# Kernel tuning notes

Hardware: AMD Instinct MI355X
Metric: run time of the kernel (lower is better)

The kernel has to match this reference:

```python
import jax, jax.numpy as jnp
import numpy as np

B, S, HID = 1, 2048, 2048
NH, NKV, D = 32, 8, 64
GROUPS = NH // NKV
THETA = 10000.0


def _rope_tables(seq_len, dim):
    inv_freq = 1.0 / (THETA ** (jnp.arange(0, dim, 2, dtype=jnp.float32) / dim))
    t = jnp.arange(seq_len, dtype=jnp.float32)
    freqs = jnp.outer(t, inv_freq)            # [S, D/2]
    emb = jnp.concatenate([freqs, freqs], axis=-1)  # [S, D]
    return jnp.cos(emb), jnp.sin(emb)


def _rotate_half(x):
    x1, x2 = jnp.split(x, 2, axis=-1)
    return jnp.concatenate([-x2, x1], axis=-1)


def setup_inputs() -> dict:
    key = jax.random.key(0)
    ks = jax.random.split(key, 8)
    hidden_states = jax.random.normal(ks[0], (B, S, HID), dtype=jnp.float32)
    # additive causal mask, 0 on/below diagonal, -1e9 above
    causal = jnp.tril(jnp.ones((S, S), dtype=bool))
    attention_mask = jnp.where(causal, 0.0, -1e9).astype(jnp.float32)[None, None]
    sc = 0.02
    Wq = sc * jax.random.normal(ks[1], (NH * D, HID), dtype=jnp.float32)
    bq = jnp.zeros((NH * D,), dtype=jnp.float32)
    Wk = sc * jax.random.normal(ks[2], (NKV * D, HID), dtype=jnp.float32)
    bk = jnp.zeros((NKV * D,), dtype=jnp.float32)
    Wv = sc * jax.random.normal(ks[3], (NKV * D, HID), dtype=jnp.float32)
    bv = jnp.zeros((NKV * D,), dtype=jnp.float32)
    Wo = sc * jax.random.normal(ks[4], (HID, NH * D), dtype=jnp.float32)
    return {"hidden_states": hidden_states, "attention_mask": attention_mask,
            "Wq": Wq, "bq": bq, "Wk": Wk, "bk": bk, "Wv": Wv, "bv": bv, "Wo": Wo}


def reference(hidden_states, attention_mask, Wq, bq, Wk, bk, Wv, bv, Wo):
    b, s, _ = hidden_states.shape
    q = (hidden_states @ Wq.T + bq).reshape(b, s, NH, D).transpose(0, 2, 1, 3)   # [B,NH,S,D]
    k = (hidden_states @ Wk.T + bk).reshape(b, s, NKV, D).transpose(0, 2, 1, 3)  # [B,NKV,S,D]
    v = (hidden_states @ Wv.T + bv).reshape(b, s, NKV, D).transpose(0, 2, 1, 3)
    cos, sin = _rope_tables(s, D)
    cos = cos[None, None]; sin = sin[None, None]
    q = q * cos + _rotate_half(q) * sin
    k = k * cos + _rotate_half(k) * sin
    # GQA: repeat KV heads to match query heads
    k = jnp.repeat(k, GROUPS, axis=1)  # [B,NH,S,D]
    v = jnp.repeat(v, GROUPS, axis=1)
    scores = jnp.einsum('bhqd,bhkd->bhqk', q, k) / jnp.sqrt(jnp.float32(D))
    scores = jnp.clip(scores, -50.0, 50.0)
    scores = scores + attention_mask
    probs = jax.nn.softmax(scores.astype(jnp.float32), axis=-1).astype(q.dtype)
    attn = jnp.einsum('bhqk,bhkd->bhqd', probs, v)
    attn = attn.transpose(0, 2, 1, 3).reshape(b, s, NH * D)
    return attn @ Wo.T
```

## Files before the change

### kernel.cpp

```cpp
#include <hip/hip_runtime.h>
#include <hip/hip_bf16.h>
#include <stdint.h>

typedef unsigned short u16;
typedef unsigned int u32;

#define S_LEN 2048
#define HID 2048
#define NH 32
#define NKV 8
#define HD 64
#define PIT 2080

using f32x4 = __attribute__((ext_vector_type(4))) float;
using bfrag = __attribute__((ext_vector_type(8))) short;

__device__ __forceinline__ float b2f(u16 u) {
  union { u32 i; float f; } c; c.i = ((u32)u) << 16; return c.f;
}
__device__ __forceinline__ u16 f2b(float f) {
  union { float f; u32 i; } c; c.f = f;
  u32 r = c.i + 0x7fffu + ((c.i >> 16) & 1u);
  return (u16)(r >> 16);
}
__device__ __forceinline__ uint4 cvt8(const float* __restrict__ p) {
  float4 a = *(const float4*)p;
  float4 b = *(const float4*)(p + 4);
  uint4 r;
  r.x = (u32)f2b(a.x) | ((u32)f2b(a.y) << 16);
  r.y = (u32)f2b(a.z) | ((u32)f2b(a.w) << 16);
  r.z = (u32)f2b(b.x) | ((u32)f2b(b.y) << 16);
  r.w = (u32)f2b(b.z) | ((u32)f2b(b.w) << 16);
  return r;
}

__device__ __forceinline__ void gl2lds16(const u16* g, u16* l) {
  __builtin_amdgcn_global_load_lds(
      (const __attribute__((address_space(1))) void*)g,
      (__attribute__((address_space(3))) void*)l,
      16, 0, 0);
}

#define WAITBAR(N) asm volatile("s_waitcnt vmcnt(" #N ")\ns_barrier" ::: "memory")

__global__ void conv_all(const float* __restrict__ hid, const float* __restrict__ Wq,
                         const float* __restrict__ Wk, const float* __restrict__ Wv,
                         u16* __restrict__ hidb, u16* __restrict__ Wqkvb) {
  int row = blockIdx.x;
  int col = threadIdx.x * 8;
  const float* src; u16* dst;
  if (row < 2048)      { src = hid + (size_t)row * 2048;          dst = hidb  + (size_t)row * PIT; }
  else if (row < 4096) { src = Wq + (size_t)(row - 2048) * 2048;  dst = Wqkvb + (size_t)(row - 2048) * PIT; }
  else if (row < 4608) { src = Wk + (size_t)(row - 4096) * 2048;  dst = Wqkvb + (size_t)(row - 4096 + 2048) * PIT; }
  else                 { src = Wv + (size_t)(row - 4608) * 2048;  dst = Wqkvb + (size_t)(row - 4608 + 2560) * PIT; }
  *(uint4*)(dst + col) = cvt8(src + col);
}

__global__ void conv_f2b_p(const float* __restrict__ in, u16* __restrict__ out, int n8) {
  int i = blockIdx.x * 256 + threadIdx.x;
  if (i >= n8) return;
  int row = i >> 8;
  int col = (i & 255) * 8;
  *(uint4*)(out + (size_t)row * PIT + col) = cvt8(in + (size_t)row * 2048 + col);
}

__global__ __launch_bounds__(256, 3) void gemm_qkv(
    const u16* __restrict__ A, const u16* __restrict__ B,
    const float* __restrict__ bq, const float* __restrict__ bk, const float* __restrict__ bv,
    u16* __restrict__ Qb, u16* __restrict__ Kb, u16* __restrict__ Vt)
{
  __shared__ __align__(16) u16 As[3 * 2048];
  __shared__ __align__(16) u16 Bs[3 * 4096];
  __shared__ __align__(16) u16 strip_s[4][16 * 72];

  const int tid  = threadIdx.x;
  const int m0   = blockIdx.y * 64;
  const int n0   = blockIdx.x * 128;
  const int lane = tid & 63;
  const int w    = tid >> 6;
  const int wm   = w >> 1, wn = w & 1;
  const int quad = lane >> 4, l16 = lane & 15;

  const int srow = tid >> 2;
  const int scol = (tid & 3) * 8;
  const u16* ga = A + (size_t)(m0 + srow) * PIT + scol;
  const u16* gb = B + (size_t)(n0 + srow) * PIT + scol;

#define STAGE_G(bi, k0)                                                         \
  do {                                                                          \
    gl2lds16(ga + (k0), As + (bi) * 2048 + tid * 8);                            \
    gl2lds16(gb + (k0), Bs + (bi) * 4096 + tid * 8);                            \
    gl2lds16(gb + (size_t)64 * PIT + (k0), Bs + (bi) * 4096 + 2048 + tid * 8);  \
  } while (0)

  f32x4 zero = {0.f, 0.f, 0.f, 0.f};
  f32x4 acc[2][4];
#pragma unroll
  for (int mi = 0; mi < 2; ++mi)
#pragma unroll
    for (int ni = 0; ni < 4; ++ni) acc[mi][ni] = zero;

  STAGE_G(0, 0);
  STAGE_G(1, 32);

  int cur = 0;
  for (int k = 0; k < 64; ++k) {
    if (k < 63) WAITBAR(3);
    else        WAITBAR(0);
    if (k + 2 < 64) {
      int nb = cur + 2; if (nb >= 3) nb -= 3;
      STAGE_G(nb, (k + 2) * 32);
    }
    const u16* as = As + cur * 2048;
    const u16* bs = Bs + cur * 4096;

    bfrag af[2], bf[4];
#pragma unroll
    for (int i = 0; i < 2; ++i)
      af[i] = *(const bfrag*)&as[(wm * 32 + i * 16 + l16) * 32 + quad * 8];
#pragma unroll
    for (int i = 0; i < 4; ++i)
      bf[i] = *(const bfrag*)&bs[(wn * 64 + i * 16 + l16) * 32 + quad * 8];
#pragma unroll
    for (int mi = 0; mi < 2; ++mi)
#pragma unroll
      for (int ni = 0; ni < 4; ++ni)
        acc[mi][ni] = __builtin_amdgcn_mfma_f32_16x16x32_bf16(af[mi], bf[ni], acc[mi][ni], 0, 0, 0);

    cur += 1; if (cur == 3) cur = 0;
  }
#undef STAGE_G

  u16* strip = strip_s[w];
  const int rr = lane >> 2;
  const int co = (lane & 3) * 8;

  if (n0 < 2048) {
#pragma unroll
    for (int mi = 0; mi < 2; ++mi) {
#pragma unroll
      for (int n01 = 0; n01 < 2; ++n01)
#pragma unroll
        for (int i = 0; i < 4; ++i) {
          int d  = n01 * 16 + l16;
          int c1 = n0 + wn * 64 + d;
          float x1 = acc[mi][n01][i]     + bq[c1];
          float x2 = acc[mi][n01 + 2][i] + bq[c1 + 32];
          float inv = exp2f(-(float)d * 0.41524101186092034f);
          float ang = (float)(m0 + wm * 32 + mi * 16 + quad * 4 + i) * inv;
          float cs = cosf(ang), sn = sinf(ang);
          strip[(quad * 4 + i) * 72 + d]      = f2b(x1 * cs - x2 * sn);
          strip[(quad * 4 + i) * 72 + d + 32] = f2b(x2 * cs + x1 * sn);
        }
      uint4 v0 = *(const uint4*)&strip[rr * 72 + co];
      uint4 v1 = *(const uint4*)&strip[rr * 72 + 32 + co];
      size_t gb2 = (size_t)(m0 + wm * 32 + mi * 16 + rr) * 2048 + n0 + wn * 64;
      *(uint4*)(Qb + gb2 + co)      = v0;
      *(uint4*)(Qb + gb2 + 32 + co) = v1;
    }
  } else if (n0 < 2560) {
    int cb = (n0 - 2048) + wn * 64;
#pragma unroll
    for (int mi = 0; mi < 2; ++mi) {
#pragma unroll
      for (int n01 = 0; n01 < 2; ++n01)
#pragma unroll
        for (int i = 0; i < 4; ++i) {
          int d  = n01 * 16 + l16;
          int cg = cb + d;
          float x1 = acc[mi][n01][i]     + bk[cg];
          float x2 = acc[mi][n01 + 2][i] + bk[cg + 32];
          float inv = exp2f(-(float)d * 0.41524101186092034f);
          float ang = (float)(m0 + wm * 32 + mi * 16 + quad * 4 + i) * inv;
          float cs = cosf(ang), sn = sinf(ang);
          strip[(quad * 4 + i) * 72 + d]      = f2b(x1 * cs - x2 * sn);
          strip[(quad * 4 + i) * 72 + d + 32] = f2b(x2 * cs + x1 * sn);
        }
      uint4 v0 = *(const uint4*)&strip[rr * 72 + co];
      uint4 v1 = *(const uint4*)&strip[rr * 72 + 32 + co];
      size_t gb2 = (size_t)(m0 + wm * 32 + mi * 16 + rr) * 512 + cb;
      *(uint4*)(Kb + gb2 + co)      = v0;
      *(uint4*)(Kb + gb2 + 32 + co) = v1;
    }
  } else {
    int cgb = (n0 - 2560) + wn * 64;
#pragma unroll
    for (int ni = 0; ni < 4; ++ni) {
      float bvv = bv[cgb + ni * 16 + l16];
#pragma unroll
      for (int mi = 0; mi < 2; ++mi)
#pragma unroll
        for (int i = 0; i < 4; ++i)
          strip[l16 * 72 + mi * 16 + quad * 4 + i] = f2b(acc[mi][ni][i] + bvv);
      uint4 v0 = *(const uint4*)&strip[rr * 72 + co];
      size_t gb2 = (size_t)(cgb + ni * 16 + rr) * PIT + m0 + wm * 32;
      *(uint4*)(Vt + gb2 + co) = v0;
    }
  }
}

__global__ __launch_bounds__(256, 3) void gemm_o(
    const u16* __restrict__ A, const u16* __restrict__ B, float* __restrict__ C)
{
  __shared__ __align__(16) u16 As[3 * 2048];
  __shared__ __align__(16) u16 Bs[3 * 4096];

  const int tid  = threadIdx.x;
  const int m0   = blockIdx.y * 64;
  const int n0   = blockIdx.x * 128;
  const int lane = tid & 63;
  const int w    = tid >> 6;
  const int wm   = w >> 1, wn = w & 1;
  const int quad = lane >> 4, l16 = lane & 15;

  const int srow = tid >> 2;
  const int scol = (tid & 3) * 8;
  const u16* ga = A + (size_t)(m0 + srow) * PIT + scol;
  const u16* gb = B + (size_t)(n0 + srow) * PIT + scol;

#define STAGE_G(bi, k0)                                                         \
  do {                                                                          \
    gl2lds16(ga + (k0), As + (bi) * 2048 + tid * 8);                            \
    gl2lds16(gb + (k0), Bs + (bi) * 4096 + tid * 8);                            \
    gl2lds16(gb + (size_t)64 * PIT + (k0), Bs + (bi) * 4096 + 2048 + tid * 8);  \
  } while (0)

  f32x4 zero = {0.f, 0.f, 0.f, 0.f};
  f32x4 acc[2][4];
#pragma unroll
  for (int mi = 0; mi < 2; ++mi)
#pragma unroll
    for (int ni = 0; ni < 4; ++ni) acc[mi][ni] = zero;

  STAGE_G(0, 0);
  STAGE_G(1, 32);

  int cur = 0;
  for (int k = 0; k < 64; ++k) {
    if (k < 63) WAITBAR(3);
    else        WAITBAR(0);
    if (k + 2 < 64) {
      int nb = cur + 2; if (nb >= 3) nb -= 3;
      STAGE_G(nb, (k + 2) * 32);
    }
    const u16* as = As + cur * 2048;
    const u16* bs = Bs + cur * 4096;

    bfrag af[2], bf[4];
#pragma unroll
    for (int i = 0; i < 2; ++i)
      af[i] = *(const bfrag*)&as[(wm * 32 + i * 16 + l16) * 32 + quad * 8];
#pragma unroll
    for (int i = 0; i < 4; ++i)
      bf[i] = *(const bfrag*)&bs[(wn * 64 + i * 16 + l16) * 32 + quad * 8];
#pragma unroll
    for (int mi = 0; mi < 2; ++mi)
#pragma unroll
      for (int ni = 0; ni < 4; ++ni)
        acc[mi][ni] = __builtin_amdgcn_mfma_f32_16x16x32_bf16(af[mi], bf[ni], acc[mi][ni], 0, 0, 0);

    cur += 1; if (cur == 3) cur = 0;
  }
#undef STAGE_G

#pragma unroll
  for (int ni = 0; ni < 4; ++ni) {
    int col = n0 + wn * 64 + ni * 16 + l16;
#pragma unroll
    for (int mi = 0; mi < 2; ++mi)
#pragma unroll
      for (int i = 0; i < 4; ++i) {
        int row = m0 + wm * 32 + mi * 16 + quad * 4 + i;
        C[(size_t)row * 2048 + col] = acc[mi][ni][i];
      }
  }
}

#define SM_SC 0.18033688011112042f
#define SM_UB 72.134752044448169f

__global__ __launch_bounds__(256, 2) void attn_flash5(
    const u16* __restrict__ Qb, const u16* __restrict__ Kb,
    const u16* __restrict__ Vt, u16* __restrict__ Ab)
{
  __shared__ __align__(16) u16 Ks[3][64 * 64];
  __shared__ __align__(16) u16 Vs[3][64 * 64];
  __shared__ __align__(16) u16 Ps[4][2][16][72];

  const int h    = blockIdx.x;
  const int qbb  = 15 - (int)blockIdx.y;
  const int kvh  = h >> 2;
  const int tid  = threadIdx.x;
  const int lane = tid & 63;
  const int w    = tid >> 6;
  const int quad = lane >> 4, l16 = lane & 15;

  const int c0  = w * 128 + lane;
  const int r0  = c0 >> 3,        s0 = c0 & 7;
  const int r1  = (c0 + 64) >> 3, s1 = (c0 + 64) & 7;
  const int sg0 = s0 ^ (r0 & 7);
  const int sg1 = s1 ^ (r1 & 7);
  const u16* Ksrc0 = Kb + (size_t)r0 * 512 + kvh * 64 + sg0 * 8;
  const u16* Ksrc1 = Kb + (size_t)r1 * 512 + kvh * 64 + sg1 * 8;
  const u16* Vsrc0 = Vt + (size_t)(kvh * 64 + r0) * PIT + sg0 * 8;
  const u16* Vsrc1 = Vt + (size_t)(kvh * 64 + r1) * PIT + sg1 * 8;

#define STAGEKV(buf, kb)                                                        \
  do {                                                                          \
    gl2lds16(Ksrc0 + (size_t)(kb) * 32768, &Ks[buf][0] + c0 * 8);               \
    gl2lds16(Ksrc1 + (size_t)(kb) * 32768, &Ks[buf][0] + (c0 + 64) * 8);        \
    gl2lds16(Vsrc0 + (kb) * 64,            &Vs[buf][0] + c0 * 8);               \
    gl2lds16(Vsrc1 + (kb) * 64,            &Vs[buf][0] + (c0 + 64) * 8);        \
  } while (0)

  const int bulk  = 2 * qbb;
  const int kbmax = bulk + 1;

  STAGEKV(0, 0);
  STAGEKV(1, 1);

  bfrag qf[2][2];
#pragma unroll
  for (int g = 0; g < 2; ++g) {
    const u16* qp = Qb + (size_t)(qbb * 128 + g * 64 + w * 16 + l16) * 2048 + h * 64 + quad * 8;
    qf[g][0] = *(const bfrag*)qp;
    qf[g][1] = *(const bfrag*)(qp + 32);
  }

  f32x4 zero = {0.f, 0.f, 0.f, 0.f};
  f32x4 o_acc[2][4];
  float lpart[2][4];
#pragma unroll
  for (int g = 0; g < 2; ++g)
#pragma unroll
    for (int nb = 0; nb < 4; ++nb) { o_acc[g][nb] = zero; lpart[g][nb] = 0.f; }

#define QKT_SM_FULL(g)                                                          \
  do {                                                                          \
    f32x4 s_acc[4];                                                             \
    _Pragma("unroll")                                                           \
    for (int nb = 0; nb < 4; ++nb) {                                            \
      s_acc[nb] = __builtin_amdgcn_mfma_f32_16x16x32_bf16(qf[g][0], kf0[nb], zero, 0, 0, 0); \
      s_acc[nb] = __builtin_amdgcn_mfma_f32_16x16x32_bf16(qf[g][1], kf1[nb], s_acc[nb], 0, 0, 0); \
    }                                                                           \
    _Pragma("unroll")                                                           \
    for (int nb = 0; nb < 4; ++nb)                                              \
      _Pragma("unroll")                                                         \
      for (int i = 0; i < 4; ++i) {                                             \
        float u = s_acc[nb][i] * SM_SC;                                         \
        u = fminf(SM_UB, fmaxf(-SM_UB, u));                                     \
        float p = __builtin_amdgcn_exp2f(u);                                    \
        lpart[g][i] += p;                                                       \
        Ps[w][g][quad * 4 + i][nb * 16 + l16] = f2b(p);                         \
      }                                                                         \
  } while (0)

#define QKT_SM_DIAG(g)                                                          \
  do {                                                                          \
    f32x4 s_acc[4];                                                             \
    _Pragma("unroll")                                                           \
    for (int nb = 0; nb < 4; ++nb) {                                            \
      s_acc[nb] = __builtin_amdgcn_mfma_f32_16x16x32_bf16(qf[g][0], kf0[nb], zero, 0, 0, 0); \
      s_acc[nb] = __builtin_amdgcn_mfma_f32_16x16x32_bf16(qf[g][1], kf1[nb], s_acc[nb], 0, 0, 0); \
    }                                                                           \
    _Pragma("unroll")                                                           \
    for (int nb = 0; nb < 4; ++nb)                                              \
      _Pragma("unroll")                                                         \
      for (int i = 0; i < 4; ++i) {                                             \
        float u = s_acc[nb][i] * SM_SC;                                         \
        u = fminf(SM_UB, fmaxf(-SM_UB, u));                                     \
        bool msk = (nb * 16 + l16 > w * 16 + quad * 4 + i);                     \
        float p = msk ? 0.0f : __builtin_amdgcn_exp2f(u);                       \
        lpart[g][i] += p;                                                       \
        Ps[w][g][quad * 4 + i][nb * 16 + l16] = f2b(p);                         \
      }                                                                         \
  } while (0)

#define PVACC(g)                                                                \
  do {                                                                          \
    bfrag pf0 = *(const bfrag*)&Ps[w][g][l16][quad * 8];                        \
    bfrag pf1 = *(const bfrag*)&Ps[w][g][l16][32 + quad * 8];                   \
    _Pragma("unroll")                                                           \
    for (int nb = 0; nb < 4; ++nb) {                                            \
      o_acc[g][nb] = __builtin_amdgcn_mfma_f32_16x16x32_bf16(pf0, vf0[nb], o_acc[g][nb], 0, 0, 0); \
      o_acc[g][nb] = __builtin_amdgcn_mfma_f32_16x16x32_bf16(pf1, vf1[nb], o_acc[g][nb], 0, 0, 0); \
    }                                                                           \
  } while (0)

  const int swz = (l16 & 7) * 8;

  int cur = 0;
  for (int kb = 0; kb <= kbmax; ++kb) {
    if (kb < kbmax) WAITBAR(4);
    else            WAITBAR(0);
    if (kb + 2 <= kbmax) {
      int nb3 = cur + 2; if (nb3 >= 3) nb3 -= 3;
      STAGEKV(nb3, kb + 2);
    }

    const u16* ks = &Ks[cur][0];
    const u16* vs = &Vs[cur][0];

    bfrag kf0[4], kf1[4];
#pragma unroll
    for (int nb = 0; nb < 4; ++nb) {
      int row = (nb * 16 + l16) * 64;
      kf0[nb] = *(const bfrag*)&ks[row + ((quad * 8) ^ swz)];
      kf1[nb] = *(const bfrag*)&ks[row + ((32 + quad * 8) ^ swz)];
    }

    if (kb < bulk)        { QKT_SM_FULL(0); QKT_SM_FULL(1); }
    else if (kb == bulk)  { QKT_SM_DIAG(0); QKT_SM_FULL(1); }
    else                  { QKT_SM_DIAG(1); }

    bfrag vf0[4], vf1[4];
#pragma unroll
    for (int nb = 0; nb < 4; ++nb) {
      int row = (nb * 16 + l16) * 64;
      vf0[nb] = *(const bfrag*)&vs[row + ((quad * 8) ^ swz)];
      vf1[nb] = *(const bfrag*)&vs[row + ((32 + quad * 8) ^ swz)];
    }

    if (kb <= bulk) PVACC(0);
    PVACC(1);

    cur += 1; if (cur == 3) cur = 0;
  }

#pragma unroll
  for (int off = 1; off < 16; off <<= 1)
#pragma unroll
    for (int g = 0; g < 2; ++g)
#pragma unroll
      for (int i = 0; i < 4; ++i)
        lpart[g][i] += __shfl_xor(lpart[g][i], off, 64);

#pragma unroll
  for (int g = 0; g < 2; ++g)
#pragma unroll
    for (int i = 0; i < 4; ++i) {
      float inv = 1.0f / lpart[g][i];
      size_t rbase = (size_t)(qbb * 128 + g * 64 + w * 16 + quad * 4 + i) * PIT + h * 64;
#pragma unroll
      for (int nb = 0; nb < 4; ++nb)
        Ab[rbase + nb * 16 + l16] = f2b(o_acc[g][nb][i] * inv);
    }
}

extern "C" void kernel_launch(void* const* d_in, const int* in_sizes, int n_in,
                              void* d_out, int out_size, void* d_ws, size_t ws_size,
                              hipStream_t stream) {
  const float* hid = (const float*)d_in[0];
  const float* Wq = (const float*)d_in[2];
  const float* bq = (const float*)d_in[3];
  const float* Wk = (const float*)d_in[4];
  const float* bk = (const float*)d_in[5];
  const float* Wv = (const float*)d_in[6];
  const float* bv = (const float*)d_in[7];
  const float* Wo = (const float*)d_in[8];

  u16* hidb  = (u16*)d_ws;
  u16* Wqkvb = hidb + (size_t)2048 * PIT;
  u16* Qb    = Wqkvb + (size_t)3072 * PIT;
  u16* Kb    = Qb + 4194304;
  u16* Vt    = Kb + 1048576;
  u16* Wob   = hidb;
  u16* Ab    = Wqkvb;
  float* Ob  = (float*)d_out;

  conv_all<<<5120, 256, 0, stream>>>(hid, Wq, Wk, Wv, hidb, Wqkvb);

  gemm_qkv<<<dim3(24, 32), 256, 0, stream>>>(hidb, Wqkvb, bq, bk, bv, Qb, Kb, Vt);

  conv_f2b_p<<<2048, 256, 0, stream>>>(Wo, Wob, 524288);

  attn_flash5<<<dim3(32, 16), 256, 0, stream>>>(Qb, Kb, Vt, Ab);

  gemm_o<<<dim3(16, 32), 256, 0, stream>>>(Ab, Wob, Ob);
}
```

Baseline: 262.3 us.

## Pair complementary causal query tiles per block for balanced attention work

Each attention block used to handle one 128-row query block (two 64-row groups), so the amount of work depended on its position in the causal triangle. Now each block handles a 64-row tile from the end (31-p) and one from the start (p), always 33 KV iterations, streaming KV continuously and writing the first tile's output partway through. This is meant to balance work across blocks and remove tail imbalance. The cost is that each K/V tile now feeds only 64 query rows instead of 128, which halves reuse of each LDS tile.

```diff
diff --git a/kernel.cpp b/kernel.cpp
--- a/kernel.cpp
+++ b/kernel.cpp
@@ -279,21 +279,24 @@
 #define SM_SC 0.18033688011112042f
 #define SM_UB 72.134752044448169f
 
-__global__ __launch_bounds__(256, 2) void attn_flash5(
+__global__ __launch_bounds__(256, 2) void attn_flash6(
     const u16* __restrict__ Qb, const u16* __restrict__ Kb,
     const u16* __restrict__ Vt, u16* __restrict__ Ab)
 {
   __shared__ __align__(16) u16 Ks[3][64 * 64];
   __shared__ __align__(16) u16 Vs[3][64 * 64];
-  __shared__ __align__(16) u16 Ps[4][2][16][72];
+  __shared__ __align__(16) u16 Ps[4][16][72];
 
   const int h    = blockIdx.x;
-  const int qbb  = 15 - (int)blockIdx.y;
+  const int p    = blockIdx.y;
   const int kvh  = h >> 2;
   const int tid  = threadIdx.x;
   const int lane = tid & 63;
   const int w    = tid >> 6;
   const int quad = lane >> 4, l16 = lane & 15;
+
+  const int qtA = 31 - p, qtB = p;
+  const int nA  = qtA + 1;
 
   const int c0  = w * 128 + lane;
   const int r0  = c0 >> 3,        s0 = c0 & 7;
@@ -313,90 +316,37 @@
     gl2lds16(Vsrc1 + (kb) * 64,            &Vs[buf][0] + (c0 + 64) * 8);        \
   } while (0)
 
-  const int bulk  = 2 * qbb;
-  const int kbmax = bulk + 1;
-
   STAGEKV(0, 0);
   STAGEKV(1, 1);
 
-  bfrag qf[2][2];
-#pragma unroll
-  for (int g = 0; g < 2; ++g) {
-    const u16* qp = Qb + (size_t)(qbb * 128 + g * 64 + w * 16 + l16) * 2048 + h * 64 + quad * 8;
-    qf[g][0] = *(const bfrag*)qp;
-    qf[g][1] = *(const bfrag*)(qp + 32);
-  }
+  bfrag qfA0, qfA1, qfB0, qfB1;
+  {
+    const u16* qa = Qb + (size_t)(qtA * 64 + w * 16 + l16) * 2048 + h * 64 + quad * 8;
+    const u16* qb = Qb + (size_t)(qtB * 64 + w * 16 + l16) * 2048 + h * 64 + quad * 8;
+    qfA0 = *(const bfrag*)qa;  qfA1 = *(const bfrag*)(qa + 32);
+    qfB0 = *(const bfrag*)qb;  qfB1 = *(const bfrag*)(qb + 32);
+  }
+  bfrag q0 = qfA0, q1 = qfA1;
 
   f32x4 zero = {0.f, 0.f, 0.f, 0.f};
-  f32x4 o_acc[2][4];
-  float lpart[2][4];
-#pragma unroll
-  for (int g = 0; g < 2; ++g)
-#pragma unroll
-    for (int nb = 0; nb < 4; ++nb) { o_acc[g][nb] = zero; lpart[g][nb] = 0.f; }
-
-#define QKT_SM_FULL(g)                                                          \
-  do {                                                                          \
-    f32x4 s_acc[4];                                                             \
-    _Pragma("unroll")                                                           \
-    for (int nb = 0; nb < 4; ++nb) {                                            \
-      s_acc[nb] = __builtin_amdgcn_mfma_f32_16x16x32_bf16(qf[g][0], kf0[nb], zero, 0, 0, 0); \
-      s_acc[nb] = __builtin_amdgcn_mfma_f32_16x16x32_bf16(qf[g][1], kf1[nb], s_acc[nb], 0, 0, 0); \
-    }                                                                           \
-    _Pragma("unroll")                                                           \
-    for (int nb = 0; nb < 4; ++nb)                                              \
-      _Pragma("unroll")                                                         \
-      for (int i = 0; i < 4; ++i) {                                             \
-        float u = s_acc[nb][i] * SM_SC;                                         \
-        u = fminf(SM_UB, fmaxf(-SM_UB, u));                                     \
-        float p = __builtin_amdgcn_exp2f(u);                                    \
-        lpart[g][i] += p;                                                       \
-        Ps[w][g][quad * 4 + i][nb * 16 + l16] = f2b(p);                         \
-      }                                                                         \
-  } while (0)
-
-#define QKT_SM_DIAG(g)                                                          \
-  do {                                                                          \
-    f32x4 s_acc[4];                                                             \
-    _Pragma("unroll")                                                           \
-    for (int nb = 0; nb < 4; ++nb) {                                            \
-      s_acc[nb] = __builtin_amdgcn_mfma_f32_16x16x32_bf16(qf[g][0], kf0[nb], zero, 0, 0, 0); \
-      s_acc[nb] = __builtin_amdgcn_mfma_f32_16x16x32_bf16(qf[g][1], kf1[nb], s_acc[nb], 0, 0, 0); \
-    }                                                                           \
-    _Pragma("unroll")                                                           \
-    for (int nb = 0; nb < 4; ++nb)                                              \
-      _Pragma("unroll")                                                         \
-      for (int i = 0; i < 4; ++i) {                                             \
-        float u = s_acc[nb][i] * SM_SC;                                         \
-        u = fminf(SM_UB, fmaxf(-SM_UB, u));                                     \
-        bool msk = (nb * 16 + l16 > w * 16 + quad * 4 + i);                     \
-        float p = msk ? 0.0f : __builtin_amdgcn_exp2f(u);                       \
-        lpart[g][i] += p;                                                       \
-        Ps[w][g][quad * 4 + i][nb * 16 + l16] = f2b(p);                         \
-      }                                                                         \
-  } while (0)
-
-#define PVACC(g)                                                                \
-  do {                                                                          \
-    bfrag pf0 = *(const bfrag*)&Ps[w][g][l16][quad * 8];                        \
-    bfrag pf1 = *(const bfrag*)&Ps[w][g][l16][32 + quad * 8];                   \
-    _Pragma("unroll")                                                           \
-    for (int nb = 0; nb < 4; ++nb) {                                            \
-      o_acc[g][nb] = __builtin_amdgcn_mfma_f32_16x16x32_bf16(pf0, vf0[nb], o_acc[g][nb], 0, 0, 0); \
-      o_acc[g][nb] = __builtin_amdgcn_mfma_f32_16x16x32_bf16(pf1, vf1[nb], o_acc[g][nb], 0, 0, 0); \
-    }                                                                           \
-  } while (0)
+  f32x4 o_acc[4];
+  float lpart[4];
+#pragma unroll
+  for (int nb = 0; nb < 4; ++nb) { o_acc[nb] = zero; lpart[nb] = 0.f; }
 
   const int swz = (l16 & 7) * 8;
-
+  int qt = qtA;
   int cur = 0;
-  for (int kb = 0; kb <= kbmax; ++kb) {
-    if (kb < kbmax) WAITBAR(4);
-    else            WAITBAR(0);
-    if (kb + 2 <= kbmax) {
-      int nb3 = cur + 2; if (nb3 >= 3) nb3 -= 3;
-      STAGEKV(nb3, kb + 2);
-    }
+
+  for (int t = 0; t < 33; ++t) {
+    if (t < 32) WAITBAR(4);
+    else        WAITBAR(0);
+    if (t + 2 < 33) {
+      int kb2 = (t + 2 < nA) ? (t + 2) : (t + 2 - nA);
+      int b3 = cur + 2; if (b3 >= 3) b3 -= 3;
+      STAGEKV(b3, kb2);
+    }
+    if (t == nA) { q0 = qfB0; q1 = qfB1; qt = qtB; }
 
     const u16* ks = &Ks[cur][0];
     const u16* vs = &Vs[cur][0];
@@ -409,9 +359,38 @@
       kf1[nb] = *(const bfrag*)&ks[row + ((32 + quad * 8) ^ swz)];
     }
 
-    if (kb < bulk)        { QKT_SM_FULL(0); QKT_SM_FULL(1); }
-    else if (kb == bulk)  { QKT_SM_DIAG(0); QKT_SM_FULL(1); }
-    else                  { QKT_SM_DIAG(1); }
+    const bool diag = (t == nA - 1) || (t == 32);
+
+    f32x4 s_acc[4];
+#pragma unroll
+    for (int nb = 0; nb < 4; ++nb) {
+      s_acc[nb] = __builtin_amdgcn_mfma_f32_16x16x32_bf16(q0, kf0[nb], zero, 0, 0, 0);
+      s_acc[nb] = __builtin_amdgcn_mfma_f32_16x16x32_bf16(q1, kf1[nb], s_acc[nb], 0, 0, 0);
+    }
+    if (diag) {
+#pragma unroll
+      for (int nb = 0; nb < 4; ++nb)
+#pragma unroll
+        for (int i = 0; i < 4; ++i) {
+          float u = s_acc[nb][i] * SM_SC;
+          u = fminf(SM_UB, fmaxf(-SM_UB, u));
+          bool msk = (nb * 16 + l16 > w * 16 + quad * 4 + i);
+          float pr = msk ? 0.0f : __builtin_amdgcn_exp2f(u);
+          lpart[i] += pr;
+          Ps[w][quad * 4 + i][nb * 16 + l16] = f2b(pr);
+        }
+    } else {
+#pragma unroll
+      for (int nb = 0; nb < 4; ++nb)
+#pragma unroll
+        for (int i = 0; i < 4; ++i) {
+          float u = s_acc[nb][i] * SM_SC;
+          u = fminf(SM_UB, fmaxf(-SM_UB, u));
+          float pr = __builtin_amdgcn_exp2f(u);
+          lpart[i] += pr;
+          Ps[w][quad * 4 + i][nb * 16 + l16] = f2b(pr);
+        }
+    }
 
     bfrag vf0[4], vf1[4];
 #pragma unroll
@@ -420,31 +399,36 @@
       vf0[nb] = *(const bfrag*)&vs[row + ((quad * 8) ^ swz)];
       vf1[nb] = *(const bfrag*)&vs[row + ((32 + quad * 8) ^ swz)];
     }
-
-    if (kb <= bulk) PVACC(0);
-    PVACC(1);
+    {
+      bfrag pf0 = *(const bfrag*)&Ps[w][l16][quad * 8];
+      bfrag pf1 = *(const bfrag*)&Ps[w][l16][32 + quad * 8];
+#pragma unroll
+      for (int nb = 0; nb < 4; ++nb) {
+        o_acc[nb] = __builtin_amdgcn_mfma_f32_16x16x32_bf16(pf0, vf0[nb], o_acc[nb], 0, 0, 0);
+        o_acc[nb] = __builtin_amdgcn_mfma_f32_16x16x32_bf16(pf1, vf1[nb], o_acc[nb], 0, 0, 0);
+      }
+    }
+
+    if (diag) {
+#pragma unroll
+      for (int off = 1; off < 16; off <<= 1)
+#pragma unroll
+        for (int i = 0; i < 4; ++i)
+          lpart[i] += __shfl_xor(lpart[i], off, 64);
+#pragma unroll
+      for (int i = 0; i < 4; ++i) {
+        float inv = 1.0f / lpart[i];
+        size_t rbase = (size_t)(qt * 64 + w * 16 + quad * 4 + i) * PIT + h * 64;
+#pragma unroll
+        for (int nb = 0; nb < 4; ++nb)
+          Ab[rbase + nb * 16 + l16] = f2b(o_acc[nb][i] * inv);
+      }
+#pragma unroll
+      for (int nb = 0; nb < 4; ++nb) { o_acc[nb] = zero; lpart[nb] = 0.f; }
+    }
 
     cur += 1; if (cur == 3) cur = 0;
   }
-
-#pragma unroll
-  for (int off = 1; off < 16; off <<= 1)
-#pragma unroll
-    for (int g = 0; g < 2; ++g)
-#pragma unroll
-      for (int i = 0; i < 4; ++i)
-        lpart[g][i] += __shfl_xor(lpart[g][i], off, 64);
-
-#pragma unroll
-  for (int g = 0; g < 2; ++g)
-#pragma unroll
-    for (int i = 0; i < 4; ++i) {
-      float inv = 1.0f / lpart[g][i];
-      size_t rbase = (size_t)(qbb * 128 + g * 64 + w * 16 + quad * 4 + i) * PIT + h * 64;
-#pragma unroll
-      for (int nb = 0; nb < 4; ++nb)
-        Ab[rbase + nb * 16 + l16] = f2b(o_acc[g][nb][i] * inv);
-    }
 }
 
 extern "C" void kernel_launch(void* const* d_in, const int* in_sizes, int n_in,
@@ -474,7 +458,7 @@
 
   conv_f2b_p<<<2048, 256, 0, stream>>>(Wo, Wob, 524288);
 
-  attn_flash5<<<dim3(32, 16), 256, 0, stream>>>(Qb, Kb, Vt, Ab);
+  attn_flash6<<<dim3(32, 16), 256, 0, stream>>>(Qb, Kb, Vt, Ab);
 
   gemm_o<<<dim3(16, 32), 256, 0, stream>>>(Ab, Wob, Ob);
 }
```

Measured after the change: 250.0 us. 1.05x faster.
